# Optimization experiments

Measured on AMD Instinct MI355X. Metric: run time of the kernel, lower is better.

The kernel has to match this reference:

```python
import jax, jax.numpy as jnp
import numpy as np

N = 50000      # nodes
D = 64         # in_channels == hidden_channels
L = 3          # num_layers
DEG = 16       # avg degree
SLOPE = 0.2    # GATv2 leaky_relu negative slope (PyG default)


def setup_inputs() -> dict:
    key = jax.random.key(0)
    ks = jax.random.split(key, 8)
    x = jax.random.normal(ks[0], (N, D), dtype=jnp.float32)
    # random edges with no self loops (PyG GATv2 removes then re-adds self loops)
    E = N * DEG
    dst = jax.random.randint(ks[1], (E,), 0, N)
    off = jax.random.randint(ks[2], (E,), 1, N)
    src = (dst + off) % N
    loops = jnp.arange(N)
    edge_index = jnp.stack([
        jnp.concatenate([src, loops]),   # row 0: source j
        jnp.concatenate([dst, loops]),   # row 1: target i
    ]).astype(jnp.int64)
    s = 1.0 / np.sqrt(D)
    Wl = (jax.random.normal(ks[3], (L, D, D)) * s).astype(jnp.float32)
    Wr = (jax.random.normal(ks[4], (L, D, D)) * s).astype(jnp.float32)
    att = (jax.random.normal(ks[5], (L, D)) * s).astype(jnp.float32)
    bl = jnp.zeros((L, D), jnp.float32)
    br = jnp.zeros((L, D), jnp.float32)
    bias = jnp.zeros((L, D), jnp.float32)
    return dict(x=x, edge_index=edge_index, Wl=Wl, bl=bl, Wr=Wr, br=br,
                att=att, bias=bias)


def reference(x, edge_index, Wl, bl, Wr, br, att, bias):
    src, dst = edge_index[0], edge_index[1]
    n = x.shape[0]
    for l in range(L):  # stacked GATv2 layers (structural loop, not data loop)
        xl = x @ Wl[l] + bl[l]                    # lin_l (source transform) [N,D]
        xr = x @ Wr[l] + br[l]                    # lin_r (target transform) [N,D]
        e = jax.nn.leaky_relu(xl[src] + xr[dst], SLOPE)   # [E,D]
        logits = e @ att[l]                       # [E]
        # softmax over incoming edges of each target node
        m = jax.ops.segment_max(logits, dst, num_segments=n)
        ex = jnp.exp(logits - m[dst])
        denom = jax.ops.segment_sum(ex, dst, num_segments=n)
        alpha = ex / denom[dst]                   # [E]
        x = jax.ops.segment_sum(xl[src] * alpha[:, None], dst,
                                num_segments=n) + bias[l]
        x = jax.nn.gelu(x, approximate=False)     # F.gelu (exact erf)
        # dropout p=0.0 -> no-op
    return x
```

## Files before the change

### kernel.cpp

```cpp
#include <hip/hip_runtime.h>
#include <hip/hip_bf16.h>

#define SLOPE 0.2f


__global__ __launch_bounds__(256) void k_zero(int* __restrict__ p, int n) {
    int i = blockIdx.x * 256 + threadIdx.x;
    if (i < n) p[i] = 0;
}

__global__ __launch_bounds__(256) void k_detect(const int* __restrict__ ei, int nwords,
                                                int* __restrict__ flag) {
    __shared__ int cnt;
    if (threadIdx.x == 0) cnt = 0;
    __syncthreads();
    int z = 0;
    for (int i = threadIdx.x; i < nwords; i += 256)
        if ((i & 1) && ei[i] == 0) z++;
    atomicAdd(&cnt, z);
    __syncthreads();
    if (threadIdx.x == 0) *flag = (cnt > nwords / 4) ? 1 : 0;
}

__device__ inline int esrc_at(const int* ei, int E, int f, int e) {
    return f ? ei[2 * e] : ei[e];
}
__device__ inline int edst_at(const int* ei, int E, int f, int e) {
    return f ? ei[2 * (E + e)] : ei[E + e];
}


__global__ __launch_bounds__(256) void k_hist(const int* __restrict__ ei, int E,
                                              const int* __restrict__ flag,
                                              int* __restrict__ deg) {
    int e = blockIdx.x * 256 + threadIdx.x;
    if (e < E) atomicAdd(&deg[edst_at(ei, E, *flag, e)], 1);
}

__global__ __launch_bounds__(256) void k_scan_part(const int* __restrict__ deg, int n,
                                                   int* __restrict__ parts) {
    __shared__ int s[256];
    int base = blockIdx.x * 1024;
    int sum = 0;
    for (int j = threadIdx.x; j < 1024; j += 256) {
        int i = base + j;
        sum += (i < n) ? deg[i] : 0;
    }
    s[threadIdx.x] = sum;
    __syncthreads();
    for (int off = 128; off > 0; off >>= 1) {
        if (threadIdx.x < off) s[threadIdx.x] += s[threadIdx.x + off];
        __syncthreads();
    }
    if (threadIdx.x == 0) parts[blockIdx.x] = s[0];
}

__global__ __launch_bounds__(64) void k_scan_top(int* __restrict__ parts, int NB,
                                                 int* __restrict__ rowp, int n) {
    if (threadIdx.x == 0 && blockIdx.x == 0) {
        int run = 0;
        for (int b = 0; b < NB; ++b) {
            int t = parts[b];
            parts[b] = run;
            run += t;
        }
        rowp[n] = run;
    }
}

__global__ __launch_bounds__(256) void k_scan_final(const int* __restrict__ deg, int n,
                                                    const int* __restrict__ parts,
                                                    int* __restrict__ rowp) {
    __shared__ int s[256];
    int t = threadIdx.x;
    int base = blockIdx.x * 1024 + t * 4;
    int v0 = (base + 0 < n) ? deg[base + 0] : 0;
    int v1 = (base + 1 < n) ? deg[base + 1] : 0;
    int v2 = (base + 2 < n) ? deg[base + 2] : 0;
    int v3 = (base + 3 < n) ? deg[base + 3] : 0;
    int mysum = v0 + v1 + v2 + v3;
    s[t] = mysum;
    __syncthreads();
    for (int off = 1; off < 256; off <<= 1) {
        int add = (t >= off) ? s[t - off] : 0;
        __syncthreads();
        s[t] += add;
        __syncthreads();
    }
    int excl = parts[blockIdx.x] + s[t] - mysum;
    if (base + 0 < n) rowp[base + 0] = excl;
    if (base + 1 < n) rowp[base + 1] = excl + v0;
    if (base + 2 < n) rowp[base + 2] = excl + v0 + v1;
    if (base + 3 < n) rowp[base + 3] = excl + v0 + v1 + v2;
}

__global__ __launch_bounds__(256) void k_scatter(const int* __restrict__ ei, int E,
                                                 const int* __restrict__ flag,
                                                 const int* __restrict__ rowp,
                                                 int* __restrict__ cur,
                                                 int* __restrict__ ssrc) {
    int e = blockIdx.x * 256 + threadIdx.x;
    if (e < E) {
        int f = *flag;
        int i = edst_at(ei, E, f, e);
        int pos = rowp[i] + atomicAdd(&cur[i], 1);
        ssrc[pos] = esrc_at(ei, E, f, e);
    }
}


__device__ inline void storef(float* p, size_t i, float v) { p[i] = v; }
__device__ inline void storef(__hip_bfloat16* p, size_t i, float v) {
    p[i] = __float2bfloat16(v);
}

__device__ inline void load8(const float* p, size_t row, int q, float v[8]) {
    const float4* b = reinterpret_cast<const float4*>(p + row * 64);
    float4 x = b[q * 2], y = b[q * 2 + 1];
    v[0] = x.x; v[1] = x.y; v[2] = x.z; v[3] = x.w;
    v[4] = y.x; v[5] = y.y; v[6] = y.z; v[7] = y.w;
}
__device__ inline void load8(const __hip_bfloat16* p, size_t row, int q, float v[8]) {
    uint4 u = reinterpret_cast<const uint4*>(p + row * 64)[q];
    v[0] = __uint_as_float(u.x << 16);
    v[1] = __uint_as_float(u.x & 0xffff0000u);
    v[2] = __uint_as_float(u.y << 16);
    v[3] = __uint_as_float(u.y & 0xffff0000u);
    v[4] = __uint_as_float(u.z << 16);
    v[5] = __uint_as_float(u.z & 0xffff0000u);
    v[6] = __uint_as_float(u.w << 16);
    v[7] = __uint_as_float(u.w & 0xffff0000u);
}


template <typename ST, typename SR>
__global__ __launch_bounds__(256) void k_lin2(const float* __restrict__ x,
                                              const float* __restrict__ Wl,
                                              const float* __restrict__ bl,
                                              const float* __restrict__ Wr,
                                              const float* __restrict__ br,
                                              ST* __restrict__ xl,
                                              SR* __restrict__ xr, int n) {
    __shared__ float sWl[4096], sWr[4096], sbl[64], sbr[64];
    int t = threadIdx.x;
    for (int k = t; k < 4096; k += 256) {
        sWl[k] = Wl[k];
        sWr[k] = Wr[k];
    }
    if (t < 64) {
        sbl[t] = bl[t];
        sbr[t] = br[t];
    }
    __syncthreads();
    int col = t & 63;
    int rl = t >> 6;
    int ngroups = (n + 3) >> 2;
    for (int g = blockIdx.x; g < ngroups; g += gridDim.x) {
        int row = g * 4 + rl;
        if (row < n) {
            const float4* xp4 = reinterpret_cast<const float4*>(x + (size_t)row * 64);
            float al = sbl[col], ar = sbr[col];
#pragma unroll
            for (int k4 = 0; k4 < 16; ++k4) {
                float4 xv = xp4[k4];
                int kb = k4 << 2;
                al = fmaf(xv.x, sWl[((kb + 0) << 6) + col], al);
                ar = fmaf(xv.x, sWr[((kb + 0) << 6) + col], ar);
                al = fmaf(xv.y, sWl[((kb + 1) << 6) + col], al);
                ar = fmaf(xv.y, sWr[((kb + 1) << 6) + col], ar);
                al = fmaf(xv.z, sWl[((kb + 2) << 6) + col], al);
                ar = fmaf(xv.z, sWr[((kb + 2) << 6) + col], ar);
                al = fmaf(xv.w, sWl[((kb + 3) << 6) + col], al);
                ar = fmaf(xv.w, sWr[((kb + 3) << 6) + col], ar);
            }
            storef(xl, (size_t)row * 64 + col, al);
            storef(xr, (size_t)row * 64 + col, ar);
        }
    }
}

template <typename ST, typename SR>
__global__ __launch_bounds__(256) void k_gat(const ST* __restrict__ xl,
                                             const SR* __restrict__ xr,
                                             const int* __restrict__ rowp,
                                             const int* __restrict__ ssrc,
                                             const float* __restrict__ att,
                                             const float* __restrict__ bias,
                                             float* __restrict__ out, int n) {
    int wid = (blockIdx.x * 256 + threadIdx.x) >> 6;
    if (wid >= n) return;
    int lane = threadIdx.x & 63;
    int g = lane >> 3;
    int q = lane & 7;
    float a[8], r[8];
    load8(att, 0, q, a);
    load8(xr, (size_t)wid, q, r);
    int beg = rowp[wid], end = rowp[wid + 1];
    float m = -3.4e38f, denom = 0.f;
    float acc[8] = {0.f, 0.f, 0.f, 0.f, 0.f, 0.f, 0.f, 0.f};
    for (int e = beg; e < end; e += 8) {
        int rem = end - e;
        bool valid = (g < rem);
        int idx = e + (valid ? g : rem - 1);
        int s = ssrc[idx];
        float v[8];
        load8(xl, (size_t)s, q, v);
        float l = 0.f;
#pragma unroll
        for (int j = 0; j < 8; ++j) {
            float tj = v[j] + r[j];
            tj = tj > 0.f ? tj : SLOPE * tj;
            l = fmaf(a[j], tj, l);
        }
        l += __shfl_xor(l, 1);
        l += __shfl_xor(l, 2);
        l += __shfl_xor(l, 4);
        float mnew = valid ? fmaxf(m, l) : m;
        float sc = __expf(m - mnew);
        float p = valid ? __expf(l - mnew) : 0.f;
        denom = denom * sc + p;
#pragma unroll
        for (int j = 0; j < 8; ++j) acc[j] = fmaf(acc[j], sc, p * v[j]);
        m = mnew;
    }
    float mt = m;
    mt = fmaxf(mt, __shfl_xor(mt, 8));
    mt = fmaxf(mt, __shfl_xor(mt, 16));
    mt = fmaxf(mt, __shfl_xor(mt, 32));
    float sc = __expf(m - mt);
    denom *= sc;
    denom += __shfl_xor(denom, 8);
    denom += __shfl_xor(denom, 16);
    denom += __shfl_xor(denom, 32);
#pragma unroll
    for (int j = 0; j < 8; ++j) {
        acc[j] *= sc;
        acc[j] += __shfl_xor(acc[j], 8);
        acc[j] += __shfl_xor(acc[j], 16);
        acc[j] += __shfl_xor(acc[j], 32);
    }
    if (g == 0) {
        float b[8];
        load8(bias, 0, q, b);
        float inv = 1.f / denom;
        float o[8];
#pragma unroll
        for (int j = 0; j < 8; ++j) {
            float oj = acc[j] * inv + b[j];
            o[j] = 0.5f * oj * (1.0f + erff(oj * 0.70710678118654752f));
        }
        float4* ob = reinterpret_cast<float4*>(out + (size_t)wid * 64);
        ob[q * 2] = make_float4(o[0], o[1], o[2], o[3]);
        ob[q * 2 + 1] = make_float4(o[4], o[5], o[6], o[7]);
    }
}


template <typename ST, typename SR>
static void run_layers(const float* x0, const float* Wl, const float* bl,
                       const float* Wr, const float* br, const float* att,
                       const float* bias, ST* xl, SR* xr, const int* rowp,
                       const int* ssrc, float* xout, int N, hipStream_t stream) {
    int gat_grid = (N + 3) / 4;
    for (int l = 0; l < 3; ++l) {
        const float* xin = (l == 0) ? x0 : xout;
        k_lin2<ST, SR><<<2048, 256, 0, stream>>>(
            xin, Wl + (size_t)l * 4096, bl + (size_t)l * 64,
            Wr + (size_t)l * 4096, br + (size_t)l * 64, xl, xr, N);
        k_gat<ST, SR><<<gat_grid, 256, 0, stream>>>(xl, xr, rowp, ssrc,
                                                    att + (size_t)l * 64,
                                                    bias + (size_t)l * 64, xout, N);
    }
}

extern "C" void kernel_launch(void* const* d_in, const int* in_sizes, int n_in,
                              void* d_out, int out_size, void* d_ws, size_t ws_size,
                              hipStream_t stream) {
    (void)n_in;
    (void)out_size;
    const float* x0 = (const float*)d_in[0];
    const int* ei = (const int*)d_in[1];
    const float* Wl = (const float*)d_in[2];
    const float* bl = (const float*)d_in[3];
    const float* Wr = (const float*)d_in[4];
    const float* br = (const float*)d_in[5];
    const float* att = (const float*)d_in[6];
    const float* bias = (const float*)d_in[7];

    int N = in_sizes[0] / 64;
    int E = in_sizes[1] / 2;
    size_t ND = (size_t)N * 64;

    char* w = (char*)d_ws;
    int* flag = (int*)w;  w += 256;
    int* parts = (int*)w; w += 4096;
    int* rowp = (int*)w;  w += ((size_t)N + 8) * 4;
    int* deg = (int*)w;   w += ((size_t)N + 8) * 4;
    int* cur = (int*)w;   w += ((size_t)N + 8) * 4;
    int* ssrc = (int*)w;  w += ((size_t)E + 8) * 4;
    size_t head = (size_t)(w - (char*)d_ws);

    bool big = (ws_size >= head + ND * 2 + ND * 4 + 4096);

    int NB = (N + 1023) / 1024;
    int neb = (E + 255) / 256;
    int nz2 = (2 * (N + 8) + 255) / 256;

    k_detect<<<1, 256, 0, stream>>>(ei, 4096, flag);
    k_zero<<<nz2, 256, 0, stream>>>(deg, 2 * (N + 8));
    k_hist<<<neb, 256, 0, stream>>>(ei, E, flag, deg);
    k_scan_part<<<NB, 256, 0, stream>>>(deg, N, parts);
    k_scan_top<<<1, 64, 0, stream>>>(parts, NB, rowp, N);
    k_scan_final<<<NB, 256, 0, stream>>>(deg, N, parts, rowp);
    k_scatter<<<neb, 256, 0, stream>>>(ei, E, flag, rowp, cur, ssrc);

    float* xout = (float*)d_out;
    if (big) {
        __hip_bfloat16* xl = (__hip_bfloat16*)w;
        float* xr = (float*)(w + ND * 2);
        run_layers<__hip_bfloat16, float>(x0, Wl, bl, Wr, br, att, bias, xl, xr,
                                          rowp, ssrc, xout, N, stream);
    } else {
        __hip_bfloat16* xl = (__hip_bfloat16*)w;
        __hip_bfloat16* xr = xl + ND;
        run_layers<__hip_bfloat16, __hip_bfloat16>(x0, Wl, bl, Wr, br, att, bias,
                                                   xl, xr, rowp, ssrc, xout, N,
                                                   stream);
    }
}
```

Before: 313.3 us.

## Record per-edge rank in histogram, drop scatter atomics, store source ids as uint16

The histogram pass now saves each edge's atomic return value as its rank within its destination segment. The scatter pass then writes directly to rowp+rank without a second atomic counter array, and the cur array and its zeroing go away. When N fits in 16 bits the CSR source indices are stored as unsigned short, halving index traffic in the three GAT layers. This costs an extra E-sized rank buffer write and read.

```diff
diff --git a/kernel.cpp b/kernel.cpp
--- a/kernel.cpp
+++ b/kernel.cpp
@@ -32,9 +32,10 @@
 
 __global__ __launch_bounds__(256) void k_hist(const int* __restrict__ ei, int E,
                                               const int* __restrict__ flag,
-                                              int* __restrict__ deg) {
+                                              int* __restrict__ deg,
+                                              int* __restrict__ rank) {
     int e = blockIdx.x * 256 + threadIdx.x;
-    if (e < E) atomicAdd(&deg[edst_at(ei, E, *flag, e)], 1);
+    if (e < E) rank[e] = atomicAdd(&deg[edst_at(ei, E, *flag, e)], 1);
 }
 
 __global__ __launch_bounds__(256) void k_scan_part(const int* __restrict__ deg, int n,
@@ -94,17 +95,17 @@
     if (base + 3 < n) rowp[base + 3] = excl + v0 + v1 + v2;
 }
 
+template <typename IT>
 __global__ __launch_bounds__(256) void k_scatter(const int* __restrict__ ei, int E,
                                                  const int* __restrict__ flag,
                                                  const int* __restrict__ rowp,
-                                                 int* __restrict__ cur,
-                                                 int* __restrict__ ssrc) {
+                                                 const int* __restrict__ rank,
+                                                 IT* __restrict__ ssrc) {
     int e = blockIdx.x * 256 + threadIdx.x;
     if (e < E) {
         int f = *flag;
         int i = edst_at(ei, E, f, e);
-        int pos = rowp[i] + atomicAdd(&cur[i], 1);
-        ssrc[pos] = esrc_at(ei, E, f, e);
+        ssrc[rowp[i] + rank[e]] = (IT)esrc_at(ei, E, f, e);
     }
 }
 
@@ -179,11 +180,11 @@
     }
 }
 
-template <typename ST, typename SR>
+template <typename ST, typename SR, typename IT>
 __global__ __launch_bounds__(256) void k_gat(const ST* __restrict__ xl,
                                              const SR* __restrict__ xr,
                                              const int* __restrict__ rowp,
-                                             const int* __restrict__ ssrc,
+                                             const IT* __restrict__ ssrc,
                                              const float* __restrict__ att,
                                              const float* __restrict__ bias,
                                              float* __restrict__ out, int n) {
@@ -202,7 +203,7 @@
         int rem = end - e;
         bool valid = (g < rem);
         int idx = e + (valid ? g : rem - 1);
-        int s = ssrc[idx];
+        int s = (int)ssrc[idx];
         float v[8];
         load8(xl, (size_t)s, q, v);
         float l = 0.f;
@@ -256,20 +257,21 @@
 }
 
 
-template <typename ST, typename SR>
+template <typename ST, typename SR, typename IT>
 static void run_layers(const float* x0, const float* Wl, const float* bl,
                        const float* Wr, const float* br, const float* att,
                        const float* bias, ST* xl, SR* xr, const int* rowp,
-                       const int* ssrc, float* xout, int N, hipStream_t stream) {
+                       const IT* ssrc, float* xout, int N, hipStream_t stream) {
     int gat_grid = (N + 3) / 4;
     for (int l = 0; l < 3; ++l) {
         const float* xin = (l == 0) ? x0 : xout;
         k_lin2<ST, SR><<<2048, 256, 0, stream>>>(
             xin, Wl + (size_t)l * 4096, bl + (size_t)l * 64,
             Wr + (size_t)l * 4096, br + (size_t)l * 64, xl, xr, N);
-        k_gat<ST, SR><<<gat_grid, 256, 0, stream>>>(xl, xr, rowp, ssrc,
-                                                    att + (size_t)l * 64,
-                                                    bias + (size_t)l * 64, xout, N);
+        k_gat<ST, SR, IT><<<gat_grid, 256, 0, stream>>>(xl, xr, rowp, ssrc,
+                                                        att + (size_t)l * 64,
+                                                        bias + (size_t)l * 64,
+                                                        xout, N);
     }
 }
 
@@ -292,39 +294,51 @@
     size_t ND = (size_t)N * 64;
 
     char* w = (char*)d_ws;
-    int* flag = (int*)w;  w += 256;
-    int* parts = (int*)w; w += 4096;
-    int* rowp = (int*)w;  w += ((size_t)N + 8) * 4;
-    int* deg = (int*)w;   w += ((size_t)N + 8) * 4;
-    int* cur = (int*)w;   w += ((size_t)N + 8) * 4;
-    int* ssrc = (int*)w;  w += ((size_t)E + 8) * 4;
+    int* flag = (int*)w;       w += 256;
+    int* parts = (int*)w;      w += 4096;
+    int* rowp = (int*)w;       w += ((size_t)N + 8) * 4;
+    int* deg = (int*)w;        w += ((size_t)N + 8) * 4;
+    int* rank = (int*)w;       w += ((size_t)E + 8) * 4;
+    unsigned short* ssrc16 = (unsigned short*)w;
+    int* ssrc32 = (int*)w;     w += ((size_t)E + 8) * 4;
     size_t head = (size_t)(w - (char*)d_ws);
 
     bool big = (ws_size >= head + ND * 2 + ND * 4 + 4096);
+    bool small_ids = (N <= 65535);
 
     int NB = (N + 1023) / 1024;
     int neb = (E + 255) / 256;
-    int nz2 = (2 * (N + 8) + 255) / 256;
+    int nzb = (N + 255) / 256;
 
     k_detect<<<1, 256, 0, stream>>>(ei, 4096, flag);
-    k_zero<<<nz2, 256, 0, stream>>>(deg, 2 * (N + 8));
-    k_hist<<<neb, 256, 0, stream>>>(ei, E, flag, deg);
+    k_zero<<<nzb, 256, 0, stream>>>(deg, N);
+    k_hist<<<neb, 256, 0, stream>>>(ei, E, flag, deg, rank);
     k_scan_part<<<NB, 256, 0, stream>>>(deg, N, parts);
     k_scan_top<<<1, 64, 0, stream>>>(parts, NB, rowp, N);
     k_scan_final<<<NB, 256, 0, stream>>>(deg, N, parts, rowp);
-    k_scatter<<<neb, 256, 0, stream>>>(ei, E, flag, rowp, cur, ssrc);
+    if (small_ids)
+        k_scatter<unsigned short><<<neb, 256, 0, stream>>>(ei, E, flag, rowp, rank, ssrc16);
+    else
+        k_scatter<int><<<neb, 256, 0, stream>>>(ei, E, flag, rowp, rank, ssrc32);
 
     float* xout = (float*)d_out;
     if (big) {
         __hip_bfloat16* xl = (__hip_bfloat16*)w;
         float* xr = (float*)(w + ND * 2);
-        run_layers<__hip_bfloat16, float>(x0, Wl, bl, Wr, br, att, bias, xl, xr,
-                                          rowp, ssrc, xout, N, stream);
+        if (small_ids)
+            run_layers<__hip_bfloat16, float, unsigned short>(
+                x0, Wl, bl, Wr, br, att, bias, xl, xr, rowp, ssrc16, xout, N, stream);
+        else
+            run_layers<__hip_bfloat16, float, int>(
+                x0, Wl, bl, Wr, br, att, bias, xl, xr, rowp, ssrc32, xout, N, stream);
     } else {
         __hip_bfloat16* xl = (__hip_bfloat16*)w;
         __hip_bfloat16* xr = xl + ND;
-        run_layers<__hip_bfloat16, __hip_bfloat16>(x0, Wl, bl, Wr, br, att, bias,
-                                                   xl, xr, rowp, ssrc, xout, N,
-                                                   stream);
-    }
-}
+        if (small_ids)
+            run_layers<__hip_bfloat16, __hip_bfloat16, unsigned short>(
+                x0, Wl, bl, Wr, br, att, bias, xl, xr, rowp, ssrc16, xout, N, stream);
+        else
+            run_layers<__hip_bfloat16, __hip_bfloat16, int>(
+                x0, Wl, bl, Wr, br, att, bias, xl, xr, rowp, ssrc32, xout, N, stream);
+    }
+}
```

Result: faster. 277.1 us (-11.6%).
